# Performance work log

Measured on AMD Instinct MI355X. Metric: run time of the kernel, lower is better.

Reference implementation:

```python
import jax, jax.numpy as jnp
import numpy as np

B, S, D_IN, D_OUT = 2, 4096, 512, 512


def setup_inputs() -> dict:
    key = jax.random.key(0)
    k1, k2, k3, k4 = jax.random.split(key, 4)
    x = jax.random.normal(k1, (B, S, D_IN), dtype=jnp.float32)
    # weights stored as [d_in, d_out] so projection is x @ W
    W_query = jax.random.normal(k2, (D_IN, D_OUT), dtype=jnp.float32) * (D_IN ** -0.5)
    W_key = jax.random.normal(k3, (D_IN, D_OUT), dtype=jnp.float32) * (D_IN ** -0.5)
    W_value = jax.random.normal(k4, (D_IN, D_OUT), dtype=jnp.float32) * (D_IN ** -0.5)
    return {"x": x, "W_query": W_query, "W_key": W_key, "W_value": W_value}


def reference(x, W_query, W_key, W_value):
    # Faithful to source: masked_fill is called non-in-place and its result
    # discarded, so NO causal mask is actually applied. Dropout prob = 0.0.
    d_out = W_query.shape[-1]
    q = jnp.einsum('bsi,io->bso', x, W_query)  # [B,S,D_OUT]
    k = jnp.einsum('bsi,io->bso', x, W_key)
    v = jnp.einsum('bsi,io->bso', x, W_value)
    scores = jnp.einsum('bqd,bkd->bqk', q, k) / jnp.sqrt(jnp.float32(d_out))
    weights = jax.nn.softmax(scores, axis=-1)  # [B,S,S]
    context = jnp.einsum('bqk,bkd->bqd', weights, v)  # [B,S,D_OUT]
    return context
```

## Files before the change

### kernel.cpp

```cpp
#include <hip/hip_runtime.h>
#include <cstdint>
#include <cstddef>

typedef unsigned short u16;
typedef __attribute__((ext_vector_type(8))) short bf16x8;
typedef __attribute__((ext_vector_type(4))) float f32x4;

struct alignas(8) u16x4_t { u16 x, y, z, w; };

__device__ __forceinline__ u16 f2bf(float f) {
  uint32_t u = __builtin_bit_cast(uint32_t, f);
  u += 0x7FFFu + ((u >> 16) & 1u);
  return (u16)(u >> 16);
}
__device__ __forceinline__ float bf2f(u16 h) {
  uint32_t u = ((uint32_t)h) << 16;
  return __builtin_bit_cast(float, u);
}

__device__ __forceinline__ void g2l16(const u16* g, u16* l) {
  __builtin_amdgcn_global_load_lds(
      (const __attribute__((address_space(1))) void*)g,
      (__attribute__((address_space(3))) void*)l, 16, 0, 0);
}

#define S_WAITCNT_VM(N) \
  __builtin_amdgcn_s_waitcnt((((N) & 0xF)) | (0x7 << 4) | (0xF << 8) | ((((N) >> 4) & 3) << 14))
#define S_WAITCNT_LGKM0 __builtin_amdgcn_s_waitcnt(0xC07F)

template <int DEPTH, int BM, int BN>
__device__ __forceinline__ void gemm_bt_pipe(
    const u16* __restrict__ A, const u16* __restrict__ Bt,
    int lda, int ldb, int kIters, int m0, int n0,
    u16* sh, f32x4 (&acc)[BM / 32][BN / 32], int tid) {
  constexpr int MI = BM / 32;
  constexpr int NI = BN / 32;
  constexpr int T = (BM + BN) / 64;
  constexpr int SLOT = (BM + BN) * 32;
  const int lane = tid & 63, wave = tid >> 6;
  const int wm = wave >> 1, wn = wave & 1, lr = lane & 15, quad = lane >> 4;

  const u16* gp[T];
#pragma unroll
  for (int t = 0; t < T; ++t) {
    const int c = t * 256 + wave * 64 + lane;
    if (c < BM * 4) {
      const int r = c >> 2;
      const int s = (c & 3) ^ ((r >> 1) & 3);
      gp[t] = A + (size_t)(m0 + r) * lda + s * 8;
    } else {
      const int cb = c - BM * 4;
      const int r = cb >> 2;
      const int s = (cb & 3) ^ ((r >> 1) & 3);
      gp[t] = Bt + (size_t)(n0 + r) * ldb + s * 8;
    }
  }
  const int wo = wave * 512;

  auto issue = [&](int slot, int kb) {
    u16* s = sh + slot * SLOT;
#pragma unroll
    for (int t = 0; t < T; ++t)
      g2l16(gp[t] + kb, s + t * 2048 + wo);
  };

#pragma unroll
  for (int p = 0; p < DEPTH; ++p)
    issue(p, (p < kIters ? p : kIters - 1) * 32);

  const int xq = (quad ^ ((lr >> 1) & 3)) * 8;
  const int arow = wm * (BM / 2) + lr;
  const int brow = wn * (BN / 2) + lr;

  bf16x8 af[MI], b0[NI], b1[NI];
  S_WAITCNT_VM(T * (DEPTH - 1));
  __builtin_amdgcn_s_barrier();
#pragma unroll
  for (int ni = 0; ni < NI; ++ni)
    b0[ni] = *(const bf16x8*)(sh + BM * 32 + ((brow + ni * 16) * 32 + xq));
#pragma unroll
  for (int mi = 0; mi < MI; ++mi)
    af[mi] = *(const bf16x8*)(sh + ((arow + mi * 16) * 32 + xq));

  auto step = [&](int kt, bf16x8 (&bc)[NI], bf16x8 (&bn)[NI]) {
    S_WAITCNT_VM(T * (DEPTH - 2));
    __builtin_amdgcn_s_barrier();
    const int nx = (kt + 1 < kIters) ? kt + 1 : kIters - 1;
    u16* s1 = sh + (nx % DEPTH) * SLOT;
#pragma unroll
    for (int ni = 0; ni < NI; ++ni)
      bn[ni] = *(const bf16x8*)(s1 + BM * 32 + ((brow + ni * 16) * 32 + xq));
    __builtin_amdgcn_s_setprio(1);
#pragma unroll
    for (int mi = 0; mi < MI; ++mi) {
#pragma unroll
      for (int ni = 0; ni < NI; ++ni)
        acc[mi][ni] = __builtin_amdgcn_mfma_f32_16x16x32_bf16(af[mi], bc[ni], acc[mi][ni], 0, 0, 0);
      af[mi] = *(const bf16x8*)(s1 + ((arow + mi * 16) * 32 + xq));
    }
    __builtin_amdgcn_s_setprio(0);
    __builtin_amdgcn_s_barrier();
    const int kn = kt + DEPTH;
    issue(kn % DEPTH, (kn < kIters ? kn : kIters - 1) * 32);
  };

  for (int kt = 0; kt + 2 <= kIters; kt += 2) {
    step(kt, b0, b1);
    step(kt + 1, b1, b0);
  }
}

template <int BM, int BN>
__device__ __forceinline__ void gemm_bt_8w_4ph(
    const u16* __restrict__ A, const u16* __restrict__ Bt,
    int lda, int ldb, int kIters, int m0, int n0,
    u16* sh, f32x4 (&acc)[BM / 32][BN / 64]) {
  constexpr int T = (BM + BN) / 128;
  constexpr int SLOT = (BM + BN) * 32;
  const int tid = threadIdx.x;
  const int lane = tid & 63, wave = tid >> 6;
  const int wm = wave >> 2, wn = wave & 3, lr = lane & 15, quad = lane >> 4;

  const u16* gp[T];
#pragma unroll
  for (int t = 0; t < T; ++t) {
    const int c = t * 512 + wave * 64 + lane;
    if (c < BM * 4) {
      const int r = c >> 2;
      const int s = (c & 3) ^ ((r >> 1) & 3);
      gp[t] = A + (size_t)(m0 + r) * lda + s * 8;
    } else {
      const int cb = c - BM * 4;
      const int r = cb >> 2;
      const int s = (cb & 3) ^ ((r >> 1) & 3);
      gp[t] = Bt + (size_t)(n0 + r) * ldb + s * 8;
    }
  }
  const int wo = wave * 512;

#pragma unroll
  for (int p = 0; p < 2; ++p)
#pragma unroll
    for (int t = 0; t < T; ++t)
      g2l16(gp[t] + p * 32, sh + p * SLOT + t * 4096 + wo);
  S_WAITCNT_VM(4);
  __builtin_amdgcn_s_barrier();

  const int xq = (quad ^ ((lr >> 1) & 3)) * 8;
  const int abase = (wm * (BM / 2) + lr) * 32 + xq;
  const int bbase = BM * 32 + (wn * (BN / 4) + lr) * 32 + xq;

  int si = 0, s2 = 2;
  for (int kt = 0; kt < kIters; ++kt) {
    u16* slot = sh + si * SLOT;
    const int kn = kt + 2;
    const int kb = (kn < kIters ? kn : kIters - 1) * 32;
    u16* st = sh + s2 * SLOT + wo;

    bf16x8 a0[4], b0[4];
#pragma unroll
    for (int i = 0; i < 4; ++i)
      a0[i] = *(const bf16x8*)(slot + abase + i * 512);
#pragma unroll
    for (int j = 0; j < 4; ++j)
      b0[j] = *(const bf16x8*)(slot + bbase + j * 512);
    g2l16(gp[0] + kb, st);
    g2l16(gp[1] + kb, st + 4096);
    __builtin_amdgcn_s_barrier();
    S_WAITCNT_LGKM0;
    __builtin_amdgcn_s_setprio(1);
#pragma unroll
    for (int i = 0; i < 4; ++i)
#pragma unroll
      for (int j = 0; j < 4; ++j)
        acc[i][j] = __builtin_amdgcn_mfma_f32_16x16x32_bf16(a0[i], b0[j], acc[i][j], 0, 0, 0);
    __builtin_amdgcn_s_setprio(0);
    __builtin_amdgcn_s_barrier();
#pragma unroll
    for (int i = 0; i < 4; ++i)
      a0[i] = *(const bf16x8*)(slot + abase + (4 + i) * 512);
    g2l16(gp[2] + kb, st + 8192);
    g2l16(gp[3] + kb, st + 12288);
    __builtin_amdgcn_s_barrier();
    S_WAITCNT_LGKM0;
    __builtin_amdgcn_s_setprio(1);
#pragma unroll
    for (int i = 0; i < 4; ++i)
#pragma unroll
      for (int j = 0; j < 4; ++j)
        acc[4 + i][j] = __builtin_amdgcn_mfma_f32_16x16x32_bf16(a0[i], b0[j], acc[4 + i][j], 0, 0, 0);
    __builtin_amdgcn_s_setprio(0);
    S_WAITCNT_VM(4);
    __builtin_amdgcn_s_barrier();
    si = si == 2 ? 0 : si + 1;
    s2 = s2 == 2 ? 0 : s2 + 1;
  }
}

#define ZERO_ACC4(acc)                        \
  _Pragma("unroll") for (int mi = 0; mi < 4; ++mi) \
  _Pragma("unroll") for (int ni = 0; ni < 4; ++ni) \
      acc[mi][ni] = f32x4{0.f, 0.f, 0.f, 0.f};

template <int MI>
__device__ __forceinline__ void epilogue_ct16(
    const f32x4 (&acc)[MI][4], u16* __restrict__ base, int m0w, int n0w,
    int ld, int lane, bool do_exp, float scale, float* rs) {
  const int lr = lane & 15, quad = lane >> 4;
  const int j = quad >> 1, par = quad & 1;
#pragma unroll
  for (int mp = 0; mp < MI / 2; ++mp) {
#pragma unroll
    for (int ni = 0; ni < 4; ++ni) {
      uint32_t p0[2], p1[2];
#pragma unroll
      for (int h = 0; h < 2; ++h) {
        const f32x4 v = acc[mp * 2 + h][ni];
        float e0, e1, e2, e3;
        if (do_exp) {
          e0 = __expf(v[0] * scale); e1 = __expf(v[1] * scale);
          e2 = __expf(v[2] * scale); e3 = __expf(v[3] * scale);
        } else {
          e0 = v[0]; e1 = v[1]; e2 = v[2]; e3 = v[3];
        }
        const u16 h0 = f2bf(e0), h1 = f2bf(e1), h2 = f2bf(e2), h3 = f2bf(e3);
        p0[h] = (uint32_t)h0 | ((uint32_t)h1 << 16);
        p1[h] = (uint32_t)h2 | ((uint32_t)h3 << 16);
        if (rs) rs[ni] += bf2f(h0) + bf2f(h1) + bf2f(h2) + bf2f(h3);
      }
      const uint32_t s0 = par ? p0[0] : p0[1];
      const uint32_t s1 = par ? p1[0] : p1[1];
      const uint32_t r0 = (uint32_t)__shfl_xor((int)s0, 16);
      const uint32_t r1 = (uint32_t)__shfl_xor((int)s1, 16);
      uint4 st;
      if (!par) { st.x = p0[0]; st.y = p1[0]; st.z = r0;    st.w = r1;    }
      else      { st.x = r0;    st.y = r1;    st.z = p0[1]; st.w = p1[1]; }
      const int m = m0w + 16 * (mp * 2 + par) + 8 * j;
      const int n = n0w + ni * 16 + lr;
      *(uint4*)(base + (size_t)n * ld + m) = st;
    }
  }
}

__global__ __launch_bounds__(256) void prep_kernel(
    const float* __restrict__ x, u16* __restrict__ Xb,
    const float* __restrict__ W0, const float* __restrict__ W1,
    const float* __restrict__ W2, u16* __restrict__ Wt,
    float* __restrict__ L) {
  __shared__ float tile[32][33];
  const int id = blockIdx.x;
  if (id < 4096) {
    const int i = (id * 256 + threadIdx.x) * 4;
    const float4 v = *(const float4*)(x + i);
    u16x4_t h;
    h.x = f2bf(v.x); h.y = f2bf(v.y); h.z = f2bf(v.z); h.w = f2bf(v.w);
    *(u16x4_t*)(Xb + i) = h;
    return;
  }
  if (id >= 4864) {
    L[(id - 4864) * 256 + threadIdx.x] = 0.f;
    return;
  }
  const int t = id - 4096;
  const int wz = t >> 8, rem = t & 255;
  const float* W = wz == 0 ? W0 : (wz == 1 ? W1 : W2);
  u16* out = Wt + (size_t)wz * 512 * 512;
  const int bx = (rem & 15) * 32;
  const int by = (rem >> 4) * 32;
  const int tx = threadIdx.x & 31, ty = threadIdx.x >> 5;
#pragma unroll
  for (int i = 0; i < 32; i += 8)
    tile[ty + i][tx] = W[(size_t)(by + ty + i) * 512 + bx + tx];
  __syncthreads();
#pragma unroll
  for (int i = 0; i < 32; i += 8)
    out[(size_t)(bx + ty + i) * 512 + by + tx] = f2bf(tile[tx][ty + i]);
}

__global__ __launch_bounds__(256) void qkv_kernel(
    const u16* __restrict__ Xb, const u16* __restrict__ Wt,
    u16* __restrict__ Qb, u16* __restrict__ Kb, u16* __restrict__ Vt) {
  __shared__ u16 sh[3 * 8192];
  const int z = blockIdx.z;
  int m0, n0;
  const u16 *A, *Bt;
  if (z < 2) {
    m0 = blockIdx.y * 128;
    n0 = blockIdx.x * 128;
    A = Wt + (size_t)z * 512 * 512;
    Bt = Xb;
  } else {
    m0 = blockIdx.x * 128;
    n0 = blockIdx.y * 128;
    A = Xb;
    Bt = Wt + (size_t)2 * 512 * 512;
  }
  f32x4 acc[4][4];
  ZERO_ACC4(acc);
  gemm_bt_pipe<3, 128, 128>(A, Bt, 512, 512, 16, m0, n0, sh, acc, threadIdx.x);

  const int lane = threadIdx.x & 63, wave = threadIdx.x >> 6;
  const int wm = wave >> 1, wn = wave & 1;
  if (z < 2) {
    epilogue_ct16<4>(acc, z == 0 ? Qb : Kb, m0 + wm * 64, n0 + wn * 64, 512,
                     lane, false, 1.f, nullptr);
  } else {
    const int bb = m0 >> 12;
    epilogue_ct16<4>(acc, Vt + (size_t)bb * 512 * 4096,
                     (m0 & 4095) + wm * 64, n0 + wn * 64, 4096,
                     lane, false, 1.f, nullptr);
  }
}

__global__ __launch_bounds__(512, 2) void scores_kernel(
    const u16* __restrict__ Qb, const u16* __restrict__ Kb,
    u16* __restrict__ P, float* __restrict__ L) {
  extern __shared__ u16 sh[];
  const int id = blockIdx.x;
  const int b = id >> 8;
  const int r = id & 255;
  const int j = r >> 3;
  const int qx = (r & 7) * 2 + (j >> 4);
  const int ky = j & 15;
  const int m0 = ky * 256;
  const int n0 = qx * 256;
  f32x4 acc[8][4];
#pragma unroll
  for (int mi = 0; mi < 8; ++mi)
#pragma unroll
    for (int ni = 0; ni < 4; ++ni)
      acc[mi][ni] = f32x4{0.f, 0.f, 0.f, 0.f};
  gemm_bt_8w_4ph<256, 256>(Kb + (size_t)b * 4096 * 512,
                           Qb + (size_t)b * 4096 * 512,
                           512, 512, 16, m0, n0, sh, acc);

  const int lane = threadIdx.x & 63, wave = threadIdx.x >> 6;
  const int wm = wave >> 2, wn = wave & 3, lr = lane & 15, quad = lane >> 4;
  const float scale = 0.04419417382415922f;
  u16* Pb = P + (size_t)b * 4096 * 4096;

  float rs[4] = {0.f, 0.f, 0.f, 0.f};
  epilogue_ct16<8>(acc, Pb, m0 + wm * 128, n0 + wn * 64, 4096, lane, true,
                   scale, rs);

#pragma unroll
  for (int ni = 0; ni < 4; ++ni) {
    float v = rs[ni];
    v += __shfl_xor(v, 16);
    v += __shfl_xor(v, 32);
    if (quad == 0)
      atomicAdd(&L[b * 4096 + n0 + wn * 64 + ni * 16 + lr], v);
  }
}

__global__ __launch_bounds__(512) void pv_kernel(
    const u16* __restrict__ P, const u16* __restrict__ Vt,
    const float* __restrict__ L, float* __restrict__ out) {
  extern __shared__ u16 sh[];
  const int id = blockIdx.x;
  const int xcd = id & 7, s = id >> 3;
  const int g = s >> 2, ntile = s & 3;
  const int G = xcd + 8 * g;
  const int b = G & 1;
  const int mtile = G >> 1;
  const int m0 = mtile * 128;
  const int n0 = ntile * 128;

  const int wave8 = threadIdx.x >> 6;
  const int kg = wave8 >> 2;
  const int tid4 = threadIdx.x & 255;
  const int k0 = kg * 2048;

  f32x4 acc[4][4];
  ZERO_ACC4(acc);
  gemm_bt_pipe<3, 128, 128>(P + (size_t)b * 4096 * 4096 + k0,
                            Vt + (size_t)b * 512 * 4096 + k0,
                            4096, 4096, 64, m0, n0,
                            sh + kg * 24576, acc, tid4);

  S_WAITCNT_VM(0);
  __builtin_amdgcn_s_barrier();

  const int iw = wave8 & 3;
  const int lane = threadIdx.x & 63;
  float* cs = (float*)sh;
  float* reg = cs + iw * 4160 + lane * 65;

  if (kg == 1) {
#pragma unroll
    for (int mi = 0; mi < 4; ++mi)
#pragma unroll
      for (int ni = 0; ni < 4; ++ni)
#pragma unroll
        for (int i = 0; i < 4; ++i)
          reg[mi * 16 + ni * 4 + i] = acc[mi][ni][i];
  }
  __syncthreads();
  if (kg == 0) {
    const int wm = iw >> 1, wn = iw & 1, lr = lane & 15, quad = lane >> 4;
    const float* Lb = L + b * 4096;
#pragma unroll
    for (int mi = 0; mi < 4; ++mi) {
      const int row = m0 + wm * 64 + mi * 16 + quad * 4;
#pragma unroll
      for (int i = 0; i < 4; ++i) {
        const float rinv = 1.0f / Lb[row + i];
#pragma unroll
        for (int ni = 0; ni < 4; ++ni) {
          const int col = n0 + wn * 64 + ni * 16 + lr;
          out[(size_t)b * 2097152 + (size_t)(row + i) * 512 + col] =
              (acc[mi][ni][i] + reg[mi * 16 + ni * 4 + i]) * rinv;
        }
      }
    }
  }
}

extern "C" void kernel_launch(void* const* d_in, const int* in_sizes, int n_in,
                              void* d_out, int out_size, void* d_ws, size_t ws_size,
                              hipStream_t stream) {
  const float* x  = (const float*)d_in[0];
  const float* Wq = (const float*)d_in[1];
  const float* Wk = (const float*)d_in[2];
  const float* Wv = (const float*)d_in[3];
  float* out = (float*)d_out;
  char* ws = (char*)d_ws;
  u16* Xb = (u16*)(ws);
  u16* Qb = (u16*)(ws + 8388608);
  u16* Kb = (u16*)(ws + 16777216);
  u16* Vt = (u16*)(ws + 25165824);
  u16* Wt = (u16*)(ws + 33554432);
  u16* P  = (u16*)(ws + 35127296);
  float* L = (float*)(ws + 102236160);

  static bool attr_set = false;
  if (!attr_set) {
    hipFuncSetAttribute(reinterpret_cast<const void*>(scores_kernel),
                        hipFuncAttributeMaxDynamicSharedMemorySize, 98304);
    hipFuncSetAttribute(reinterpret_cast<const void*>(pv_kernel),
                        hipFuncAttributeMaxDynamicSharedMemorySize, 98304);
    attr_set = true;
  }

  prep_kernel<<<4896, 256, 0, stream>>>(x, Xb, Wq, Wk, Wv, Wt, L);
  qkv_kernel<<<dim3(64, 4, 3), 256, 0, stream>>>(Xb, Wt, Qb, Kb, Vt);
  scores_kernel<<<512, 512, 98304, stream>>>(Qb, Kb, P, L);
  pv_kernel<<<256, 512, 98304, stream>>>(P, Vt, L, out);
}
```

Measured before the change: 182.4 us.

## Fuse QKV, scores and PV kernels into one cooperative kernel with grid syncs

Merges the QKV projection, the scores/exp kernel and the PV kernel into one persistent cooperative kernel of 256 blocks, using grid-wide syncs between phases in place of separate launches. The QKV phase now uses 256x256 tiles on 192 blocks, and each block computes two score tiles in sequence. The aim is to remove launch gaps and kernel tails. In exchange it adds grid-sync overhead, leaves 64 blocks idle in the QKV phase, and serialises two score tiles per block, which may lower parallelism compared with the 512-block scores launch.

```diff
diff --git a/kernel.cpp b/kernel.cpp
--- a/kernel.cpp
+++ b/kernel.cpp
@@ -1,6 +1,9 @@
 #include <hip/hip_runtime.h>
+#include <hip/hip_cooperative_groups.h>
 #include <cstdint>
 #include <cstddef>
+
+namespace cg = cooperative_groups;
 
 typedef unsigned short u16;
 typedef __attribute__((ext_vector_type(8))) short bf16x8;
@@ -197,10 +200,10 @@
   }
 }
 
-#define ZERO_ACC4(acc)                        \
-  _Pragma("unroll") for (int mi = 0; mi < 4; ++mi) \
-  _Pragma("unroll") for (int ni = 0; ni < 4; ++ni) \
-      acc[mi][ni] = f32x4{0.f, 0.f, 0.f, 0.f};
+#define ZERO_ACC(acc, M)                        \
+  _Pragma("unroll") for (int mi_ = 0; mi_ < (M); ++mi_) \
+  _Pragma("unroll") for (int ni_ = 0; ni_ < 4; ++ni_) \
+      acc[mi_][ni_] = f32x4{0.f, 0.f, 0.f, 0.f};
 
 template <int MI>
 __device__ __forceinline__ void epilogue_ct16(
@@ -277,139 +280,142 @@
     out[(size_t)(bx + ty + i) * 512 + by + tx] = f2bf(tile[tx][ty + i]);
 }
 
-__global__ __launch_bounds__(256) void qkv_kernel(
+__global__ __launch_bounds__(512, 2) void fused_kernel(
     const u16* __restrict__ Xb, const u16* __restrict__ Wt,
-    u16* __restrict__ Qb, u16* __restrict__ Kb, u16* __restrict__ Vt) {
-  __shared__ u16 sh[3 * 8192];
-  const int z = blockIdx.z;
-  int m0, n0;
-  const u16 *A, *Bt;
-  if (z < 2) {
-    m0 = blockIdx.y * 128;
-    n0 = blockIdx.x * 128;
-    A = Wt + (size_t)z * 512 * 512;
-    Bt = Xb;
-  } else {
-    m0 = blockIdx.x * 128;
-    n0 = blockIdx.y * 128;
-    A = Xb;
-    Bt = Wt + (size_t)2 * 512 * 512;
-  }
-  f32x4 acc[4][4];
-  ZERO_ACC4(acc);
-  gemm_bt_pipe<3, 128, 128>(A, Bt, 512, 512, 16, m0, n0, sh, acc, threadIdx.x);
-
-  const int lane = threadIdx.x & 63, wave = threadIdx.x >> 6;
-  const int wm = wave >> 1, wn = wave & 1;
-  if (z < 2) {
-    epilogue_ct16<4>(acc, z == 0 ? Qb : Kb, m0 + wm * 64, n0 + wn * 64, 512,
-                     lane, false, 1.f, nullptr);
-  } else {
-    const int bb = m0 >> 12;
-    epilogue_ct16<4>(acc, Vt + (size_t)bb * 512 * 4096,
-                     (m0 & 4095) + wm * 64, n0 + wn * 64, 4096,
-                     lane, false, 1.f, nullptr);
-  }
-}
-
-__global__ __launch_bounds__(512, 2) void scores_kernel(
-    const u16* __restrict__ Qb, const u16* __restrict__ Kb,
-    u16* __restrict__ P, float* __restrict__ L) {
+    u16* __restrict__ Qb, u16* __restrict__ Kb, u16* __restrict__ Vt,
+    u16* __restrict__ P, float* __restrict__ L, float* __restrict__ out) {
   extern __shared__ u16 sh[];
-  const int id = blockIdx.x;
-  const int b = id >> 8;
-  const int r = id & 255;
-  const int j = r >> 3;
-  const int qx = (r & 7) * 2 + (j >> 4);
-  const int ky = j & 15;
-  const int m0 = ky * 256;
-  const int n0 = qx * 256;
-  f32x4 acc[8][4];
-#pragma unroll
-  for (int mi = 0; mi < 8; ++mi)
-#pragma unroll
-    for (int ni = 0; ni < 4; ++ni)
-      acc[mi][ni] = f32x4{0.f, 0.f, 0.f, 0.f};
-  gemm_bt_8w_4ph<256, 256>(Kb + (size_t)b * 4096 * 512,
-                           Qb + (size_t)b * 4096 * 512,
-                           512, 512, 16, m0, n0, sh, acc);
-
-  const int lane = threadIdx.x & 63, wave = threadIdx.x >> 6;
-  const int wm = wave >> 2, wn = wave & 3, lr = lane & 15, quad = lane >> 4;
-  const float scale = 0.04419417382415922f;
-  u16* Pb = P + (size_t)b * 4096 * 4096;
-
-  float rs[4] = {0.f, 0.f, 0.f, 0.f};
-  epilogue_ct16<8>(acc, Pb, m0 + wm * 128, n0 + wn * 64, 4096, lane, true,
-                   scale, rs);
-
-#pragma unroll
-  for (int ni = 0; ni < 4; ++ni) {
-    float v = rs[ni];
-    v += __shfl_xor(v, 16);
-    v += __shfl_xor(v, 32);
-    if (quad == 0)
-      atomicAdd(&L[b * 4096 + n0 + wn * 64 + ni * 16 + lr], v);
-  }
-}
-
-__global__ __launch_bounds__(512) void pv_kernel(
-    const u16* __restrict__ P, const u16* __restrict__ Vt,
-    const float* __restrict__ L, float* __restrict__ out) {
-  extern __shared__ u16 sh[];
-  const int id = blockIdx.x;
-  const int xcd = id & 7, s = id >> 3;
-  const int g = s >> 2, ntile = s & 3;
-  const int G = xcd + 8 * g;
-  const int b = G & 1;
-  const int mtile = G >> 1;
-  const int m0 = mtile * 128;
-  const int n0 = ntile * 128;
-
-  const int wave8 = threadIdx.x >> 6;
-  const int kg = wave8 >> 2;
-  const int tid4 = threadIdx.x & 255;
-  const int k0 = kg * 2048;
-
-  f32x4 acc[4][4];
-  ZERO_ACC4(acc);
-  gemm_bt_pipe<3, 128, 128>(P + (size_t)b * 4096 * 4096 + k0,
-                            Vt + (size_t)b * 512 * 4096 + k0,
-                            4096, 4096, 64, m0, n0,
-                            sh + kg * 24576, acc, tid4);
-
-  S_WAITCNT_VM(0);
+  cg::grid_group gr = cg::this_grid();
+  const int bid = blockIdx.x;
+  const int tid = threadIdx.x;
+  const int lane = tid & 63, wave = tid >> 6;
+  const int lr = lane & 15, quad = lane >> 4;
+
+  if (bid < 192) {
+    const int z = bid >> 6, w = bid & 63;
+    int m0, n0;
+    const u16 *A, *Bt;
+    if (z < 2) {
+      m0 = (w & 1) * 256;
+      n0 = (w >> 1) * 256;
+      A = Wt + (size_t)z * 262144;
+      Bt = Xb;
+    } else {
+      m0 = (w >> 1) * 256;
+      n0 = (w & 1) * 256;
+      A = Xb;
+      Bt = Wt + (size_t)2 * 262144;
+    }
+    f32x4 acc[8][4];
+    ZERO_ACC(acc, 8);
+    gemm_bt_8w_4ph<256, 256>(A, Bt, 512, 512, 16, m0, n0, sh, acc);
+
+    const int wm = wave >> 2, wn = wave & 3;
+    if (z < 2) {
+      epilogue_ct16<8>(acc, z == 0 ? Qb : Kb, m0 + wm * 128, n0 + wn * 64, 512,
+                       lane, false, 1.f, nullptr);
+    } else {
+      const int bb = m0 >> 12;
+      epilogue_ct16<8>(acc, Vt + (size_t)bb * 2097152,
+                       (m0 & 4095) + wm * 128, n0 + wn * 64, 4096,
+                       lane, false, 1.f, nullptr);
+    }
+    S_WAITCNT_VM(0);
+  }
   __builtin_amdgcn_s_barrier();
-
-  const int iw = wave8 & 3;
-  const int lane = threadIdx.x & 63;
-  float* cs = (float*)sh;
-  float* reg = cs + iw * 4160 + lane * 65;
-
-  if (kg == 1) {
-#pragma unroll
-    for (int mi = 0; mi < 4; ++mi)
-#pragma unroll
-      for (int ni = 0; ni < 4; ++ni)
-#pragma unroll
-        for (int i = 0; i < 4; ++i)
-          reg[mi * 16 + ni * 4 + i] = acc[mi][ni][i];
-  }
-  __syncthreads();
-  if (kg == 0) {
-    const int wm = iw >> 1, wn = iw & 1, lr = lane & 15, quad = lane >> 4;
-    const float* Lb = L + b * 4096;
-#pragma unroll
-    for (int mi = 0; mi < 4; ++mi) {
-      const int row = m0 + wm * 64 + mi * 16 + quad * 4;
-#pragma unroll
-      for (int i = 0; i < 4; ++i) {
-        const float rinv = 1.0f / Lb[row + i];
-#pragma unroll
-        for (int ni = 0; ni < 4; ++ni) {
-          const int col = n0 + wn * 64 + ni * 16 + lr;
-          out[(size_t)b * 2097152 + (size_t)(row + i) * 512 + col] =
-              (acc[mi][ni][i] + reg[mi * 16 + ni * 4 + i]) * rinv;
+  __threadfence();
+  gr.sync();
+
+  {
+    const int slot = bid & 7;
+    const int u = (bid >> 3) & 1;
+    const int kh = (bid >> 4) & 7;
+    const int b = bid >> 7;
+    const int qx = slot * 2 + u;
+    const int n0 = qx * 256;
+    const int wm = wave >> 2, wn = wave & 3;
+    const float scale = 0.04419417382415922f;
+    u16* Pb = P + (size_t)b * 16777216;
+
+    float rs[4] = {0.f, 0.f, 0.f, 0.f};
+#pragma unroll 1
+    for (int h = 0; h < 2; ++h) {
+      const int ky = kh + h * 8;
+      const int m0 = ky * 256;
+      f32x4 acc[8][4];
+      ZERO_ACC(acc, 8);
+      gemm_bt_8w_4ph<256, 256>(Kb + (size_t)b * 2097152,
+                               Qb + (size_t)b * 2097152,
+                               512, 512, 16, m0, n0, sh, acc);
+      epilogue_ct16<8>(acc, Pb, m0 + wm * 128, n0 + wn * 64, 4096, lane, true,
+                       scale, rs);
+      S_WAITCNT_VM(0);
+      __builtin_amdgcn_s_barrier();
+    }
+#pragma unroll
+    for (int ni = 0; ni < 4; ++ni) {
+      float v = rs[ni];
+      v += __shfl_xor(v, 16);
+      v += __shfl_xor(v, 32);
+      if (quad == 0)
+        atomicAdd(&L[b * 4096 + n0 + wn * 64 + ni * 16 + lr], v);
+    }
+  }
+  __threadfence();
+  gr.sync();
+
+  {
+    const int xcd = bid & 7, s = bid >> 3;
+    const int g2 = s >> 2, ntile = s & 3;
+    const int G = xcd + 8 * g2;
+    const int b = G & 1;
+    const int mtile = G >> 1;
+    const int m0 = mtile * 128;
+    const int n0 = ntile * 128;
+
+    const int kg = wave >> 2;
+    const int tid4 = tid & 255;
+    const int k0 = kg * 2048;
+
+    f32x4 acc[4][4];
+    ZERO_ACC(acc, 4);
+    gemm_bt_pipe<3, 128, 128>(P + (size_t)b * 16777216 + k0,
+                              Vt + (size_t)b * 2097152 + k0,
+                              4096, 4096, 64, m0, n0,
+                              sh + kg * 24576, acc, tid4);
+
+    S_WAITCNT_VM(0);
+    __builtin_amdgcn_s_barrier();
+
+    const int iw = wave & 3;
+    float* cs = (float*)sh;
+    float* reg = cs + iw * 4160 + lane * 65;
+
+    if (kg == 1) {
+#pragma unroll
+      for (int mi = 0; mi < 4; ++mi)
+#pragma unroll
+        for (int ni = 0; ni < 4; ++ni)
+#pragma unroll
+          for (int i = 0; i < 4; ++i)
+            reg[mi * 16 + ni * 4 + i] = acc[mi][ni][i];
+    }
+    __syncthreads();
+    if (kg == 0) {
+      const int wm = iw >> 1, wn = iw & 1;
+      const float* Lb = L + b * 4096;
+#pragma unroll
+      for (int mi = 0; mi < 4; ++mi) {
+        const int row = m0 + wm * 64 + mi * 16 + quad * 4;
+#pragma unroll
+        for (int i = 0; i < 4; ++i) {
+          const float rinv = 1.0f / Lb[row + i];
+#pragma unroll
+          for (int ni = 0; ni < 4; ++ni) {
+            const int col = n0 + wn * 64 + ni * 16 + lr;
+            out[(size_t)b * 2097152 + (size_t)(row + i) * 512 + col] =
+                (acc[mi][ni][i] + reg[mi * 16 + ni * 4 + i]) * rinv;
+          }
         }
       }
     }
@@ -435,15 +441,14 @@
 
   static bool attr_set = false;
   if (!attr_set) {
-    hipFuncSetAttribute(reinterpret_cast<const void*>(scores_kernel),
-                        hipFuncAttributeMaxDynamicSharedMemorySize, 98304);
-    hipFuncSetAttribute(reinterpret_cast<const void*>(pv_kernel),
+    hipFuncSetAttribute(reinterpret_cast<const void*>(fused_kernel),
                         hipFuncAttributeMaxDynamicSharedMemorySize, 98304);
     attr_set = true;
   }
 
   prep_kernel<<<4896, 256, 0, stream>>>(x, Xb, Wq, Wk, Wv, Wt, L);
-  qkv_kernel<<<dim3(64, 4, 3), 256, 0, stream>>>(Xb, Wt, Qb, Kb, Vt);
-  scores_kernel<<<512, 512, 98304, stream>>>(Qb, Kb, P, L);
-  pv_kernel<<<256, 512, 98304, stream>>>(P, Vt, L, out);
-}
+
+  void* args[] = {&Xb, &Wt, &Qb, &Kb, &Vt, &P, &L, &out};
+  hipLaunchCooperativeKernel(reinterpret_cast<void*>(fused_kernel),
+                             dim3(256), dim3(512), args, 98304, stream);
+}
```

New measurement: 328.0 us. +79.9%, slower.
